# Kernel optimization log

Measured on AMD Instinct MI355X. Metric: run time of the kernel, lower is better.

Reference implementation:

```python
import jax, jax.numpy as jnp
import numpy as np

WS = 8       # window_size
SHIFT = 4    # shift_size
HEADS = 4

def _rel_pos_index():
    coords = np.stack(np.meshgrid(np.arange(WS), np.arange(WS), indexing='ij'))
    cf = coords.reshape(2, -1)                       # (2, N)
    rel = cf[:, :, None] - cf[:, None, :]            # (2, N, N)
    rel = rel.transpose(1, 2, 0).copy()              # (N, N, 2)
    rel[:, :, 0] += WS - 1
    rel[:, :, 1] += WS - 1
    rel[:, :, 0] *= 2 * WS - 1
    return jnp.asarray(rel.sum(-1))                  # (N, N) int

REL_IDX = _rel_pos_index()

def _conv(x, w, groups=1, pad=0):
    return jax.lax.conv_general_dilated(
        x, w, (1, 1), [(pad, pad), (pad, pad)],
        feature_group_count=groups,
        dimension_numbers=('NCHW', 'OIHW', 'NCHW'))

def _dwt_haar(x):
    # single-level orthonormal Haar on non-overlapping 2x2 blocks
    B, C, H, W = x.shape
    x = x.reshape(B, C, H // 2, 2, W // 2, 2)
    a = x[:, :, :, 0, :, 0]; b = x[:, :, :, 0, :, 1]
    c = x[:, :, :, 1, :, 0]; d = x[:, :, :, 1, :, 1]
    ll = (a + b + c + d) * 0.5
    lh = (a - b + c - d) * 0.5
    hl = (a + b - c - d) * 0.5
    hh = (a - b - c + d) * 0.5
    return ll, lh, hl, hh

def _idwt_haar(ll, lh, hl, hh):
    a = (ll + lh + hl + hh) * 0.5
    b = (ll - lh + hl - hh) * 0.5
    c = (ll + lh - hl - hh) * 0.5
    d = (ll - lh - hl + hh) * 0.5
    B, C, H2, W2 = ll.shape
    x = jnp.stack([jnp.stack([a, b], -1), jnp.stack([c, d], -1)], -2)  # (B,C,H2,W2,2row,2col)
    return x.transpose(0, 1, 2, 4, 3, 5).reshape(B, C, 2 * H2, 2 * W2)

def _window_partition(x):
    B, C, H, W = x.shape
    x = x.reshape(B, C, H // WS, WS, W // WS, WS).transpose(0, 2, 4, 1, 3, 5)
    return x.reshape(-1, C, WS, WS)

def _window_reverse(w, B, H, W):
    C = w.shape[1]
    x = w.reshape(B, H // WS, W // WS, C, WS, WS).transpose(0, 3, 1, 4, 2, 5)
    return x.reshape(B, C, H, W)

def setup_inputs() -> dict:
    key = jax.random.key(0)
    ks = jax.random.split(key, 8)
    dim = 64
    s = 0.05
    return {
        'x': jax.random.normal(ks[0], (8, dim, 256, 256), jnp.float32),
        'temperature': jnp.ones((HEADS, 1, 1), jnp.float32),
        'rel_bias_table': jax.random.normal(ks[1], ((2 * WS - 1) ** 2, HEADS), jnp.float32) * 0.02,
        'w_high1': jax.random.normal(ks[2], (2 * dim, dim, 3, 3), jnp.float32) * s,
        'w_high2': jax.random.normal(ks[3], (dim, 2 * dim, 1, 1), jnp.float32) * s,
        'w_highout': jax.random.normal(ks[4], (3 * dim, dim, 3, 3), jnp.float32) * s,
        'w_qkv': jax.random.normal(ks[5], (3 * dim, dim, 1, 1), jnp.float32) * s,
        'w_dwconv': jax.random.normal(ks[6], (3 * dim, 1, 3, 3), jnp.float32) * s,
        'w_proj': jax.random.normal(ks[7], (dim, dim, 1, 1), jnp.float32) * s,
    }

def reference(x, temperature, rel_bias_table, w_high1, w_high2, w_highout, w_qkv, w_dwconv, w_proj):
    B, C, H, W = x.shape
    ll, lh, hl, hh = _dwt_haar(x)
    # high-frequency modulation of v
    filt = jax.nn.relu(_conv(jnp.concatenate([lh, hl], 1), w_high1, groups=2, pad=1))
    filt = jax.nn.relu(_conv(filt, w_high2))
    qkv = _conv(_conv(ll, w_qkv), w_dwconv, groups=3 * C, pad=1)
    v_inp = qkv[:, 2 * C:]  # note: q,k from qkv are dead in the source; q=k come from shifted LL
    v = v_inp * filt + v_inp
    xs = jnp.roll(ll, (-SHIFT, -SHIFT), (2, 3))
    qw = _window_partition(xs)
    vw = _window_partition(v)
    Bw = qw.shape[0]; hd = C // HEADS; N = WS * WS
    q = qw.reshape(Bw, HEADS, hd, N)
    vv = vw.reshape(Bw, HEADS, hd, N)
    qn = q / jnp.maximum(jnp.linalg.norm(q, axis=-2, keepdims=True), 1e-12)
    # k == q in the source, so kn == qn
    attn = jnp.einsum('bhdn,bhdm->bhnm', qn, qn)                      # (Bw,h,N,N)
    bias = rel_bias_table[REL_IDX.reshape(-1)].reshape(N, N, HEADS).transpose(2, 0, 1)
    attn = (attn + bias[None]) * temperature[None]
    attn = jax.nn.softmax(attn, axis=-1)
    out = jnp.einsum('bhdm,bhnm->bhdn', vv, attn)                     # v @ attn^T
    out = out.reshape(Bw, C, WS, WS)
    out = _window_reverse(out, B, H // 2, W // 2)
    out = jnp.roll(out, (SHIFT, SHIFT), (2, 3))
    out = _conv(out, w_proj)
    yh = jax.nn.relu(_conv(jnp.concatenate([lh, hl, hh], 1), w_highout, groups=3, pad=1))
    lh2, hl2, hh2 = yh[:, :C], yh[:, C:2 * C], yh[:, 2 * C:]
    return _idwt_haar(out, lh2, hl2, hh2)
```

## Files before the change

### kernel.cpp

```cpp
#include <hip/hip_runtime.h>
#include <cstddef>

constexpr int HP  = 128 * 128;
constexpr long long S = 8LL * 64 * HP;

using short8 = __attribute__((ext_vector_type(8))) short;
using f32x4  = __attribute__((ext_vector_type(4))) float;

__device__ __forceinline__ unsigned short f2bf(float x) {
    union { float f; unsigned int u; } v{x};
    unsigned int r = v.u + 0x7FFFu + ((v.u >> 16) & 1u);
    return (unsigned short)(r >> 16);
}

__global__ __launch_bounds__(256) void k_dwt_fused(
        const float* __restrict__ x, float* __restrict__ ll,
        unsigned short* __restrict__ Tlh, unsigned short* __restrict__ Thl,
        unsigned short* __restrict__ Thh) {
    __shared__ unsigned short tlh[64][66];
    __shared__ unsigned short thl[64][66];
    __shared__ unsigned short thh[64][66];
    int b = blockIdx.y;
    int p0 = blockIdx.x * 64;
    int i = p0 >> 7, j0 = p0 & 127;
    int tid = threadIdx.x;
    {
        int p = tid & 63, c4 = tid >> 6;
        int j = j0 + p;
        const float* xb = x + (size_t)b * 64 * 65536;
#pragma unroll
        for (int k = 0; k < 16; ++k) {
            int c = c4 * 16 + k;
            const float* xp = xb + (size_t)c * 65536;
            float2 top = *(const float2*)(xp + (2 * i) * 256 + 2 * j);
            float2 bot = *(const float2*)(xp + (2 * i + 1) * 256 + 2 * j);
            float a = top.x, bb = top.y, cc = bot.x, dd = bot.y;
            ll[((size_t)b * 64 + c) * HP + p0 + p] = (a + bb + cc + dd) * 0.5f;
            tlh[c][p] = f2bf((a - bb + cc - dd) * 0.5f);
            thl[c][p] = f2bf((a + bb - cc - dd) * 0.5f);
            thh[c][p] = f2bf((a - bb - cc + dd) * 0.5f);
        }
    }
    __syncthreads();
    {
        int c = tid & 63, pq = tid >> 6;
        size_t ob = ((size_t)b * HP + p0) * 64;
#pragma unroll
        for (int k = 0; k < 16; ++k) {
            int p = pq * 16 + k;
            Tlh[ob + (size_t)p * 64 + c] = tlh[c][p];
            Thl[ob + (size_t)p * 64 + c] = thl[c][p];
            Thh[ob + (size_t)p * 64 + c] = thh[c][p];
        }
    }
}

__global__ __launch_bounds__(256) void k_wreorder(const float* __restrict__ w,
                                                  unsigned short* __restrict__ wr, int total) {
    int idx = blockIdx.x * 256 + threadIdx.x;
    if (idx >= total) return;
    int oc = idx / 576, rem = idx - oc * 576;
    int s = rem >> 6, ic = rem & 63;
    wr[idx] = f2bf(w[(oc * 64 + ic) * 9 + s]);
}

__global__ __launch_bounds__(256) void k_bias(const float* __restrict__ table,
                                              const float* __restrict__ temp,
                                              float* __restrict__ bd) {
    int idx = blockIdx.x * 256 + threadIdx.x;
    int h = idx >> 12, m = (idx >> 6) & 63, n = idx & 63;
    int i1 = n >> 3, j1 = n & 7, i2 = m >> 3, j2 = m & 7;
    int rel = (i1 - i2 + 7) * 15 + (j1 - j2 + 7);
    bd[idx] = table[rel * 4 + h] * temp[h];
}

#define ISTR 72
__global__ __launch_bounds__(256, 2) void k_conv3x3_mfma(
        const unsigned short* __restrict__ in,
        const unsigned short* __restrict__ wr,
        float* __restrict__ out, int out_ctot) {
    __shared__ __align__(16) unsigned short lin[324 * ISTR];
    __shared__ __align__(16) unsigned short lw[64 * ISTR];

    int tid = threadIdx.x;
    int b = blockIdx.y;
    int ty0 = (blockIdx.x >> 3) * 16, tx0 = (blockIdx.x & 7) * 16;

    const unsigned short* inb = in + (size_t)b * HP * 64;
    for (int idx = tid; idx < 324 * 8; idx += 256) {
        int pr = idx >> 3, l8 = idx & 7;
        int py = pr / 18, px = pr - py * 18;
        int gy = ty0 + py - 1, gx = tx0 + px - 1;
        uint4 v = make_uint4(0, 0, 0, 0);
        if (gy >= 0 && gy < 128 && gx >= 0 && gx < 128)
            v = *(const uint4*)(inb + ((size_t)(gy * 128 + gx)) * 64 + l8 * 8);
        *(uint4*)&lin[pr * ISTR + l8 * 8] = v;
    }

    int wv = tid >> 6;
    int lane = tid & 63;
    int n16 = lane & 15, quad = lane >> 4;

    f32x4 acc[4][4];
#pragma unroll
    for (int mt = 0; mt < 4; ++mt)
#pragma unroll
        for (int nt = 0; nt < 4; ++nt) acc[mt][nt] = (f32x4){0.f, 0.f, 0.f, 0.f};

    for (int s = 0; s < 9; ++s) {
        __syncthreads();
        for (int idx = tid; idx < 512; idx += 256) {
            int oc = idx >> 3, l8 = idx & 7;
            *(uint4*)&lw[oc * ISTR + l8 * 8] =
                *(const uint4*)(wr + oc * 576 + s * 64 + l8 * 8);
        }
        __syncthreads();
        int sy = s / 3, sx = s - sy * 3;
#pragma unroll
        for (int half = 0; half < 2; ++half) {
            int ic0 = half * 32 + quad * 8;
            short8 a[4], bf[4];
#pragma unroll
            for (int mt = 0; mt < 4; ++mt)
                a[mt] = *(const short8*)&lw[(mt * 16 + n16) * ISTR + ic0];
#pragma unroll
            for (int nt = 0; nt < 4; ++nt) {
                int py = 4 * wv + nt + sy;
                int px = n16 + sx;
                bf[nt] = *(const short8*)&lin[(py * 18 + px) * ISTR + ic0];
            }
#pragma unroll
            for (int mt = 0; mt < 4; ++mt)
#pragma unroll
                for (int nt = 0; nt < 4; ++nt)
                    acc[mt][nt] = __builtin_amdgcn_mfma_f32_16x16x32_bf16(
                        a[mt], bf[nt], acc[mt][nt], 0, 0, 0);
        }
    }

    int gx = tx0 + n16;
#pragma unroll
    for (int nt = 0; nt < 4; ++nt) {
        int gy = ty0 + 4 * wv + nt;
#pragma unroll
        for (int mt = 0; mt < 4; ++mt) {
#pragma unroll
            for (int r = 0; r < 4; ++r) {
                int oc = mt * 16 + quad * 4 + r;
                out[((size_t)b * out_ctot + oc) * HP + (size_t)gy * 128 + gx] =
                    fmaxf(acc[mt][nt][r], 0.0f);
            }
        }
    }
}

template <int IC, bool RELU>
__global__ __launch_bounds__(256) void k_conv1x1(const float* __restrict__ in,
                                                 const float* __restrict__ w,
                                                 float* __restrict__ out) {
    __shared__ float wl[IC * 16];
    int tid = threadIdx.x;
    int occ = blockIdx.y, b = blockIdx.z;
    for (int idx = tid; idx < IC * 16; idx += 256) {
        int o = idx & 15, ic = idx >> 4;
        wl[idx] = w[(occ * 16 + o) * IC + ic];
    }
    __syncthreads();
    int p = blockIdx.x * 256 + tid;
    const float* inp = in + (size_t)b * IC * HP + p;
    float acc[16] = {};
    for (int ic = 0; ic < IC; ++ic) {
        float xv = inp[(size_t)ic * HP];
#pragma unroll
        for (int o = 0; o < 16; ++o) acc[o] += xv * wl[ic * 16 + o];
    }
    float* op = out + ((size_t)b * 64 + occ * 16) * HP + p;
#pragma unroll
    for (int o = 0; o < 16; ++o) op[o * HP] = RELU ? fmaxf(acc[o], 0.0f) : acc[o];
}

__global__ __launch_bounds__(256) void k_dwconv_v(const float* __restrict__ t,
                                                  const float* __restrict__ wdw,
                                                  const float* __restrict__ filt,
                                                  float* __restrict__ v) {
    long long idx = (long long)blockIdx.x * 256 + threadIdx.x;
    if (idx >= S) return;
    int j = (int)(idx & 127);
    int i = (int)((idx >> 7) & 127);
    int c = (int)((idx >> 14) & 63);
    long long bc = idx >> 14;
    const float* tp = t + bc * HP;
    const float* wp = wdw + c * 9;
    float acc = 0.0f;
#pragma unroll
    for (int ky = 0; ky < 3; ++ky) {
        int y = i + ky - 1;
        if (y < 0 || y >= 128) continue;
#pragma unroll
        for (int kx = 0; kx < 3; ++kx) {
            int x = j + kx - 1;
            if (x < 0 || x >= 128) continue;
            acc += tp[y * 128 + x] * wp[ky * 3 + kx];
        }
    }
    float f = filt[idx];
    v[idx] = acc * (1.0f + f);
}

union F16 { float4 v4[4]; float f[16]; };

__global__ __launch_bounds__(512, 4) void k_attn2(const float* __restrict__ ll,
                                                  const float* __restrict__ v,
                                                  const float* __restrict__ bd,
                                                  const float* __restrict__ temp,
                                                  const float* __restrict__ wproj,
                                                  float* __restrict__ outbuf) {
    __shared__ __align__(16) float qs[64][132];
    __shared__ __align__(16) float vs[64][132];
    __shared__ __align__(16) float inv[4][128];
    int blk = blockIdx.x;
    int wjp = blk & 7, wi = (blk >> 3) & 15, b = blk >> 7;
    int tid = threadIdx.x;

    for (int idx = tid; idx < 2048; idx += 512) {
        int pq = idx & 31, c = idx >> 5;
        int i = pq >> 2, xq = (pq & 3) * 4;
        int w = xq >> 3;
        int col = w * 64 + i * 8 + (xq & 7);
        size_t cb = ((size_t)b * 64 + c) * HP;
        int qy = (wi * 8 + i + 4) & 127;
        int qx0 = wjp * 16 + xq + 4;
        int vy = wi * 8 + i, vx0 = wjp * 16 + xq;
        float4 qv;
        if (qx0 <= 124) {
            qv = *(const float4*)(ll + cb + qy * 128 + qx0);
        } else {
            const float* lr = ll + cb + qy * 128;
            qv = make_float4(lr[qx0 & 127], lr[(qx0 + 1) & 127],
                             lr[(qx0 + 2) & 127], lr[(qx0 + 3) & 127]);
        }
        *(float4*)&qs[c][col] = qv;
        *(float4*)&vs[c][col] = *(const float4*)(v + cb + vy * 128 + vx0);
    }
    __syncthreads();

    int n = tid & 63;
    int hw = tid >> 6;
    int h = hw & 3, w = hw >> 2;
    int wc = w << 6;
    float tscale = temp[h];
    float q[16];
    float ss = 0.0f;
#pragma unroll
    for (int d = 0; d < 16; ++d) {
        q[d] = qs[h * 16 + d][wc + n];
        ss += q[d] * q[d];
    }
    float invn = 1.0f / fmaxf(sqrtf(ss), 1e-12f);
    inv[h][wc + n] = invn;
    float qsc = invn * tscale;
#pragma unroll
    for (int d = 0; d < 16; ++d) q[d] *= qsc;
    __syncthreads();

    const float* bh = bd + (h << 12) + n;
    float mx = -1e30f, sum = 0.0f;
    float acc[16] = {};

    for (int c0 = 0; c0 < 64; c0 += 16) {
        float bb[16];
#pragma unroll
        for (int mm = 0; mm < 16; ++mm) bb[mm] = bh[(c0 + mm) * 64];

        float p[16] = {};
#pragma unroll
        for (int d = 0; d < 16; ++d) {
            F16 A;
            const float4* qr = (const float4*)&qs[h * 16 + d][wc + c0];
            A.v4[0] = qr[0]; A.v4[1] = qr[1]; A.v4[2] = qr[2]; A.v4[3] = qr[3];
            float qd = q[d];
#pragma unroll
            for (int mm = 0; mm < 16; ++mm) p[mm] += qd * A.f[mm];
        }
        F16 I;
        const float4* ir = (const float4*)&inv[h][wc + c0];
        I.v4[0] = ir[0]; I.v4[1] = ir[1]; I.v4[2] = ir[2]; I.v4[3] = ir[3];
        float cm = -1e30f;
#pragma unroll
        for (int mm = 0; mm < 16; ++mm) {
            p[mm] = p[mm] * I.f[mm] + bb[mm];
            cm = fmaxf(cm, p[mm]);
        }

        float nm = fmaxf(mx, cm);
        float scale = __expf(mx - nm);
        sum *= scale;
#pragma unroll
        for (int mm = 0; mm < 16; ++mm) {
            p[mm] = __expf(p[mm] - nm);
            sum += p[mm];
        }
#pragma unroll
        for (int d = 0; d < 16; ++d) acc[d] *= scale;

#pragma unroll
        for (int d = 0; d < 16; ++d) {
            F16 V;
            const float4* vr = (const float4*)&vs[h * 16 + d][wc + c0];
            V.v4[0] = vr[0]; V.v4[1] = vr[1]; V.v4[2] = vr[2]; V.v4[3] = vr[3];
            float s = acc[d];
#pragma unroll
            for (int mm = 0; mm < 16; ++mm) s += p[mm] * V.f[mm];
            acc[d] = s;
        }
        mx = nm;
    }

    float rs = 1.0f / sum;
    __syncthreads();
#pragma unroll
    for (int d = 0; d < 16; ++d) qs[h * 16 + d][wc + n] = acc[d] * rs;
    float* wl = &vs[0][0];
    for (int idx = tid; idx < 4096; idx += 512) wl[idx] = wproj[idx];
    __syncthreads();

    int h2 = tid >> 7;
    int p2 = tid & 127;
    int i2 = p2 >> 4, xp = p2 & 15;
    int col = ((xp >> 3) << 6) + (i2 << 3) + (xp & 7);
    float po[16] = {};
    for (int ic0 = 0; ic0 < 64; ic0 += 4) {
        float x0 = qs[ic0 + 0][col];
        float x1 = qs[ic0 + 1][col];
        float x2 = qs[ic0 + 2][col];
        float x3 = qs[ic0 + 3][col];
#pragma unroll
        for (int o = 0; o < 16; ++o) {
            float4 wv = *(const float4*)&wl[(h2 * 16 + o) * 64 + ic0];
            po[o] += x0 * wv.x + x1 * wv.y + x2 * wv.z + x3 * wv.w;
        }
    }
    int oy = (wi * 8 + i2 + 4) & 127, ox = (wjp * 16 + xp + 4) & 127;
#pragma unroll
    for (int o = 0; o < 16; ++o)
        outbuf[((size_t)b * 64 + h2 * 16 + o) * HP + oy * 128 + ox] = po[o];
}

__global__ __launch_bounds__(256) void k_idwt(const float* __restrict__ ll, const float* __restrict__ lh,
                                              const float* __restrict__ hl, const float* __restrict__ hh,
                                              float* __restrict__ out) {
    long long idx2 = (long long)blockIdx.x * 256 + threadIdx.x;
    if (idx2 >= S / 2) return;
    int j2 = (int)(idx2 & 63);
    int i  = (int)((idx2 >> 6) & 127);
    long long bc = idx2 >> 13;
    long long base = bc * HP + i * 128 + 2 * j2;
    float2 L = *(const float2*)(ll + base);
    float2 A = *(const float2*)(lh + base);
    float2 Bv = *(const float2*)(hl + base);
    float2 D = *(const float2*)(hh + base);
    float a0 = (L.x + A.x + Bv.x + D.x) * 0.5f;
    float b0 = (L.x - A.x + Bv.x - D.x) * 0.5f;
    float c0 = (L.x + A.x - Bv.x - D.x) * 0.5f;
    float d0 = (L.x - A.x - Bv.x + D.x) * 0.5f;
    float a1 = (L.y + A.y + Bv.y + D.y) * 0.5f;
    float b1 = (L.y - A.y + Bv.y - D.y) * 0.5f;
    float c1 = (L.y + A.y - Bv.y - D.y) * 0.5f;
    float d1 = (L.y - A.y - Bv.y + D.y) * 0.5f;
    float* op = out + bc * 256 * 256;
    *(float4*)(op + (2 * i) * 256 + 4 * j2)     = make_float4(a0, b0, a1, b1);
    *(float4*)(op + (2 * i + 1) * 256 + 4 * j2) = make_float4(c0, d0, c1, d1);
}

extern "C" void kernel_launch(void* const* d_in, const int* in_sizes, int n_in,
                              void* d_out, int out_size, void* d_ws, size_t ws_size,
                              hipStream_t stream) {
    const float* x        = (const float*)d_in[0];
    const float* temp     = (const float*)d_in[1];
    const float* table    = (const float*)d_in[2];
    const float* w_high1  = (const float*)d_in[3];
    const float* w_high2  = (const float*)d_in[4];
    const float* w_highout= (const float*)d_in[5];
    const float* w_qkv    = (const float*)d_in[6];
    const float* w_dwconv = (const float*)d_in[7];
    const float* w_proj   = (const float*)d_in[8];
    float* out = (float*)d_out;

    float* ws = (float*)d_ws;
    float* s0 = ws + 0 * S;
    float* s1 = ws + 1 * S;
    float* s2 = ws + 2 * S;
    float* s3 = ws + 3 * S;
    float* s4 = ws + 4 * S;
    float* s5 = ws + 5 * S;
    float* s6 = ws + 6 * S;
    float* s7 = ws + 7 * S;
    float* s8 = ws + 8 * S;

    unsigned short* T_lh = (unsigned short*)s4;
    unsigned short* T_hl = (unsigned short*)s4 + S;
    unsigned short* T_hh = (unsigned short*)s5;
    unsigned short* w_r1 = (unsigned short*)s5 + S;
    unsigned short* w_r2 = w_r1 + 128 * 576;
    float* bd = (float*)(w_r2 + 192 * 576);

    const int nblk = (int)(S / 256);
    dim3 b256(256);

    dim3 dg(HP / 64, 8);
    k_dwt_fused<<<dg, b256, 0, stream>>>(x, s0, T_lh, T_hl, T_hh);

    k_wreorder<<<(128 * 576 + 255) / 256, b256, 0, stream>>>(w_high1, w_r1, 128 * 576);
    k_wreorder<<<(192 * 576 + 255) / 256, b256, 0, stream>>>(w_highout, w_r2, 192 * 576);
    k_bias<<<64, b256, 0, stream>>>(table, temp, bd);

    dim3 cg(64, 8);
    k_conv3x3_mfma<<<cg, b256, 0, stream>>>(T_lh, w_r1,            s1,            128);
    k_conv3x3_mfma<<<cg, b256, 0, stream>>>(T_hl, w_r1 + 64 * 576, s1 + 64 * HP,  128);

    dim3 g1(64, 4, 8);
    k_conv1x1<128, true><<<g1, b256, 0, stream>>>(s1, w_high2, s6);

    k_conv1x1<64, false><<<g1, b256, 0, stream>>>(s0, w_qkv + 128 * 64, s7);

    k_dwconv_v<<<nblk, b256, 0, stream>>>(s7, w_dwconv + 128 * 9, s6, s6);

    k_attn2<<<1024, dim3(512), 0, stream>>>(s0, s6, bd, temp, w_proj, s8);

    k_conv3x3_mfma<<<cg, b256, 0, stream>>>(T_lh, w_r2,             s1, 64);
    k_conv3x3_mfma<<<cg, b256, 0, stream>>>(T_hl, w_r2 + 64 * 576,  s2, 64);
    k_conv3x3_mfma<<<cg, b256, 0, stream>>>(T_hh, w_r2 + 128 * 576, s3, 64);

    k_idwt<<<(int)(S / 2 / 256), b256, 0, stream>>>(s8, s1, s2, s3, out);
}
```

Baseline: 608.3 us.

## Rewrite window attention and projection with bf16 MFMA instructions

After: 560.0 us. 1.09x faster.

```diff
diff --git a/kernel.cpp b/kernel.cpp
--- a/kernel.cpp
+++ b/kernel.cpp
@@ -11,6 +11,9 @@
     union { float f; unsigned int u; } v{x};
     unsigned int r = v.u + 0x7FFFu + ((v.u >> 16) & 1u);
     return (unsigned short)(r >> 16);
+}
+__device__ __forceinline__ unsigned int pkbf(float a, float b) {
+    return (unsigned int)f2bf(a) | ((unsigned int)f2bf(b) << 16);
 }
 
 __global__ __launch_bounds__(256) void k_dwt_fused(
@@ -207,30 +210,27 @@
     v[idx] = acc * (1.0f + f);
 }
 
-union F16 { float4 v4[4]; float f[16]; };
-
-__global__ __launch_bounds__(512, 4) void k_attn2(const float* __restrict__ ll,
-                                                  const float* __restrict__ v,
-                                                  const float* __restrict__ bd,
-                                                  const float* __restrict__ temp,
-                                                  const float* __restrict__ wproj,
-                                                  float* __restrict__ outbuf) {
-    __shared__ __align__(16) float qs[64][132];
-    __shared__ __align__(16) float vs[64][132];
-    __shared__ __align__(16) float inv[4][128];
+__global__ __launch_bounds__(512, 4) void k_attn_mfma(
+        const float* __restrict__ ll, const float* __restrict__ v,
+        const float* __restrict__ bd, const float* __restrict__ temp,
+        const float* __restrict__ wproj, float* __restrict__ outbuf) {
+    __shared__ __align__(16) unsigned char lds[71680];
+    float*          qf = (float*)lds;
+    unsigned short* al = (unsigned short*)lds;
+    unsigned short* qt = (unsigned short*)(lds + 34816);
+    unsigned short* vt = (unsigned short*)(lds + 53248);
+
     int blk = blockIdx.x;
     int wjp = blk & 7, wi = (blk >> 3) & 15, b = blk >> 7;
     int tid = threadIdx.x;
 
     for (int idx = tid; idx < 2048; idx += 512) {
-        int pq = idx & 31, c = idx >> 5;
+        int ch = idx >> 5, pq = idx & 31;
         int i = pq >> 2, xq = (pq & 3) * 4;
-        int w = xq >> 3;
-        int col = w * 64 + i * 8 + (xq & 7);
-        size_t cb = ((size_t)b * 64 + c) * HP;
+        int w = xq >> 3, j0 = xq & 7;
+        size_t cb = ((size_t)b * 64 + ch) * HP;
         int qy = (wi * 8 + i + 4) & 127;
         int qx0 = wjp * 16 + xq + 4;
-        int vy = wi * 8 + i, vx0 = wjp * 16 + xq;
         float4 qv;
         if (qx0 <= 124) {
             qv = *(const float4*)(ll + cb + qy * 128 + qx0);
@@ -239,111 +239,161 @@
             qv = make_float4(lr[qx0 & 127], lr[(qx0 + 1) & 127],
                              lr[(qx0 + 2) & 127], lr[(qx0 + 3) & 127]);
         }
-        *(float4*)&qs[c][col] = qv;
-        *(float4*)&vs[c][col] = *(const float4*)(v + cb + vy * 128 + vx0);
+        int np = w * 64 + i * 8 + j0;
+        qf[(np    ) * 68 + ch] = qv.x;
+        qf[(np + 1) * 68 + ch] = qv.y;
+        qf[(np + 2) * 68 + ch] = qv.z;
+        qf[(np + 3) * 68 + ch] = qv.w;
+        int vy = wi * 8 + i, vx0 = wjp * 16 + xq;
+        float4 vv = *(const float4*)(v + cb + vy * 128 + vx0);
+        *(uint2*)&vt[(w * 64 + ch) * 72 + i * 8 + j0] =
+            make_uint2(pkbf(vv.x, vv.y), pkbf(vv.z, vv.w));
     }
     __syncthreads();
 
-    int n = tid & 63;
-    int hw = tid >> 6;
-    int h = hw & 3, w = hw >> 2;
-    int wc = w << 6;
+    {
+        int px = tid >> 2, h = tid & 3;
+        const float* qr = qf + px * 68 + h * 16;
+        float4 q0 = *(const float4*)(qr);
+        float4 q1 = *(const float4*)(qr + 4);
+        float4 q2 = *(const float4*)(qr + 8);
+        float4 q3 = *(const float4*)(qr + 12);
+        float ss = q0.x*q0.x + q0.y*q0.y + q0.z*q0.z + q0.w*q0.w
+                 + q1.x*q1.x + q1.y*q1.y + q1.z*q1.z + q1.w*q1.w
+                 + q2.x*q2.x + q2.y*q2.y + q2.z*q2.z + q2.w*q2.w
+                 + q3.x*q3.x + q3.y*q3.y + q3.z*q3.z + q3.w*q3.w;
+        float invn = 1.0f / fmaxf(sqrtf(ss), 1e-12f);
+        unsigned short* qo = qt + px * 72 + h * 16;
+        *(uint4*)(qo)     = make_uint4(pkbf(q0.x*invn, q0.y*invn), pkbf(q0.z*invn, q0.w*invn),
+                                       pkbf(q1.x*invn, q1.y*invn), pkbf(q1.z*invn, q1.w*invn));
+        *(uint4*)(qo + 8) = make_uint4(pkbf(q2.x*invn, q2.y*invn), pkbf(q2.z*invn, q2.w*invn),
+                                       pkbf(q3.x*invn, q3.y*invn), pkbf(q3.z*invn, q3.w*invn));
+    }
+    __syncthreads();
+
+    int wv = tid >> 6, lane = tid & 63;
+    int h = wv & 3, w = wv >> 2;
+    int c = lane & 15, g = lane >> 4;
+
+    short8 Fq[4];
+#pragma unroll
+    for (int t = 0; t < 4; ++t) {
+        if (g < 2) Fq[t] = *(const short8*)&qt[(w * 64 + t * 16 + c) * 72 + h * 16 + 8 * g];
+        else       Fq[t] = (short8){0, 0, 0, 0, 0, 0, 0, 0};
+    }
+    f32x4 acc[4][4];
+#pragma unroll
+    for (int ta = 0; ta < 4; ++ta)
+#pragma unroll
+        for (int tb = 0; tb < 4; ++tb)
+            acc[ta][tb] = __builtin_amdgcn_mfma_f32_16x16x32_bf16(
+                Fq[ta], Fq[tb], (f32x4){0.f, 0.f, 0.f, 0.f}, 0, 0, 0);
+
     float tscale = temp[h];
-    float q[16];
-    float ss = 0.0f;
-#pragma unroll
-    for (int d = 0; d < 16; ++d) {
-        q[d] = qs[h * 16 + d][wc + n];
-        ss += q[d] * q[d];
-    }
-    float invn = 1.0f / fmaxf(sqrtf(ss), 1e-12f);
-    inv[h][wc + n] = invn;
-    float qsc = invn * tscale;
-#pragma unroll
-    for (int d = 0; d < 16; ++d) q[d] *= qsc;
+    const float* bp = bd + (h << 12) + c;
+    float mx[4] = {-1e30f, -1e30f, -1e30f, -1e30f};
+#pragma unroll
+    for (int ta = 0; ta < 4; ++ta)
+#pragma unroll
+        for (int tb = 0; tb < 4; ++tb)
+#pragma unroll
+            for (int r = 0; r < 4; ++r) {
+                float s = acc[ta][tb][r] * tscale + bp[(ta * 16 + 4 * g + r) * 64 + tb * 16];
+                acc[ta][tb][r] = s;
+                mx[tb] = fmaxf(mx[tb], s);
+            }
+#pragma unroll
+    for (int tb = 0; tb < 4; ++tb) {
+        mx[tb] = fmaxf(mx[tb], __shfl_xor(mx[tb], 16, 64));
+        mx[tb] = fmaxf(mx[tb], __shfl_xor(mx[tb], 32, 64));
+    }
+    float sum[4] = {0.f, 0.f, 0.f, 0.f};
+#pragma unroll
+    for (int ta = 0; ta < 4; ++ta)
+#pragma unroll
+        for (int tb = 0; tb < 4; ++tb)
+#pragma unroll
+            for (int r = 0; r < 4; ++r) {
+                float p = __expf(acc[ta][tb][r] - mx[tb]);
+                acc[ta][tb][r] = p;
+                sum[tb] += p;
+            }
+    float rs[4];
+#pragma unroll
+    for (int tb = 0; tb < 4; ++tb) {
+        sum[tb] += __shfl_xor(sum[tb], 16, 64);
+        sum[tb] += __shfl_xor(sum[tb], 32, 64);
+        rs[tb] = 1.0f / sum[tb];
+    }
+    unsigned int pk[4][4][2];
+#pragma unroll
+    for (int tb = 0; tb < 4; ++tb)
+#pragma unroll
+        for (int ta = 0; ta < 4; ++ta) {
+            pk[tb][ta][0] = pkbf(acc[ta][tb][0], acc[ta][tb][1]);
+            pk[tb][ta][1] = pkbf(acc[ta][tb][2], acc[ta][tb][3]);
+        }
+
+    short8 Va[2];
+#pragma unroll
+    for (int s = 0; s < 2; ++s)
+        Va[s] = *(const short8*)&vt[(w * 64 + h * 16 + c) * 72 + s * 32 + 8 * g];
+    int srcA = (2 * (g & 1)) * 16 + c;
+    int srcB = srcA + 16;
+    int sel = g >> 1;
+#pragma unroll
+    for (int tb = 0; tb < 4; ++tb) {
+        f32x4 po = {0.f, 0.f, 0.f, 0.f};
+#pragma unroll
+        for (int s = 0; s < 2; ++s) {
+            unsigned int a0 = __shfl(pk[tb][2 * s][0], srcA, 64);
+            unsigned int b0 = __shfl(pk[tb][2 * s + 1][0], srcA, 64);
+            unsigned int a1 = __shfl(pk[tb][2 * s][1], srcA, 64);
+            unsigned int b1 = __shfl(pk[tb][2 * s + 1][1], srcA, 64);
+            unsigned int a2 = __shfl(pk[tb][2 * s][0], srcB, 64);
+            unsigned int b2 = __shfl(pk[tb][2 * s + 1][0], srcB, 64);
+            unsigned int a3 = __shfl(pk[tb][2 * s][1], srcB, 64);
+            unsigned int b3 = __shfl(pk[tb][2 * s + 1][1], srcB, 64);
+            union { short8 s8; unsigned int u[4]; } Bf;
+            Bf.u[0] = sel ? b0 : a0;
+            Bf.u[1] = sel ? b1 : a1;
+            Bf.u[2] = sel ? b2 : a2;
+            Bf.u[3] = sel ? b3 : a3;
+            po = __builtin_amdgcn_mfma_f32_16x16x32_bf16(Va[s], Bf.s8, po, 0, 0, 0);
+        }
+        int px = (2 * tb + (c >> 3)) * 16 + w * 8 + (c & 7);
+        *(uint2*)&al[px * 72 + h * 16 + 4 * g] =
+            make_uint2(pkbf(po[0] * rs[tb], po[1] * rs[tb]),
+                       pkbf(po[2] * rs[tb], po[3] * rs[tb]));
+    }
     __syncthreads();
 
-    const float* bh = bd + (h << 12) + n;
-    float mx = -1e30f, sum = 0.0f;
-    float acc[16] = {};
-
-    for (int c0 = 0; c0 < 64; c0 += 16) {
-        float bb[16];
-#pragma unroll
-        for (int mm = 0; mm < 16; ++mm) bb[mm] = bh[(c0 + mm) * 64];
-
-        float p[16] = {};
-#pragma unroll
-        for (int d = 0; d < 16; ++d) {
-            F16 A;
-            const float4* qr = (const float4*)&qs[h * 16 + d][wc + c0];
-            A.v4[0] = qr[0]; A.v4[1] = qr[1]; A.v4[2] = qr[2]; A.v4[3] = qr[3];
-            float qd = q[d];
-#pragma unroll
-            for (int mm = 0; mm < 16; ++mm) p[mm] += qd * A.f[mm];
-        }
-        F16 I;
-        const float4* ir = (const float4*)&inv[h][wc + c0];
-        I.v4[0] = ir[0]; I.v4[1] = ir[1]; I.v4[2] = ir[2]; I.v4[3] = ir[3];
-        float cm = -1e30f;
-#pragma unroll
-        for (int mm = 0; mm < 16; ++mm) {
-            p[mm] = p[mm] * I.f[mm] + bb[mm];
-            cm = fmaxf(cm, p[mm]);
-        }
-
-        float nm = fmaxf(mx, cm);
-        float scale = __expf(mx - nm);
-        sum *= scale;
-#pragma unroll
-        for (int mm = 0; mm < 16; ++mm) {
-            p[mm] = __expf(p[mm] - nm);
-            sum += p[mm];
-        }
-#pragma unroll
-        for (int d = 0; d < 16; ++d) acc[d] *= scale;
-
-#pragma unroll
-        for (int d = 0; d < 16; ++d) {
-            F16 V;
-            const float4* vr = (const float4*)&vs[h * 16 + d][wc + c0];
-            V.v4[0] = vr[0]; V.v4[1] = vr[1]; V.v4[2] = vr[2]; V.v4[3] = vr[3];
-            float s = acc[d];
-#pragma unroll
-            for (int mm = 0; mm < 16; ++mm) s += p[mm] * V.f[mm];
-            acc[d] = s;
-        }
-        mx = nm;
-    }
-
-    float rs = 1.0f / sum;
-    __syncthreads();
-#pragma unroll
-    for (int d = 0; d < 16; ++d) qs[h * 16 + d][wc + n] = acc[d] * rs;
-    float* wl = &vs[0][0];
-    for (int idx = tid; idx < 4096; idx += 512) wl[idx] = wproj[idx];
-    __syncthreads();
-
-    int h2 = tid >> 7;
-    int p2 = tid & 127;
-    int i2 = p2 >> 4, xp = p2 & 15;
-    int col = ((xp >> 3) << 6) + (i2 << 3) + (xp & 7);
-    float po[16] = {};
-    for (int ic0 = 0; ic0 < 64; ic0 += 4) {
-        float x0 = qs[ic0 + 0][col];
-        float x1 = qs[ic0 + 1][col];
-        float x2 = qs[ic0 + 2][col];
-        float x3 = qs[ic0 + 3][col];
-#pragma unroll
-        for (int o = 0; o < 16; ++o) {
-            float4 wv = *(const float4*)&wl[(h2 * 16 + o) * 64 + ic0];
-            po[o] += x0 * wv.x + x1 * wv.y + x2 * wv.z + x3 * wv.w;
-        }
-    }
-    int oy = (wi * 8 + i2 + 4) & 127, ox = (wjp * 16 + xp + 4) & 127;
-#pragma unroll
-    for (int o = 0; o < 16; ++o)
-        outbuf[((size_t)b * 64 + h2 * 16 + o) * HP + oy * 128 + ox] = po[o];
+    int to = wv & 3, pq2 = wv >> 2;
+    short8 Wf[2];
+#pragma unroll
+    for (int s = 0; s < 2; ++s) {
+        const float* wr = wproj + (to * 16 + c) * 64 + s * 32 + 8 * g;
+        float4 wa = *(const float4*)(wr);
+        float4 wb = *(const float4*)(wr + 4);
+        union { short8 s8; unsigned int u[4]; } W;
+        W.u[0] = pkbf(wa.x, wa.y); W.u[1] = pkbf(wa.z, wa.w);
+        W.u[2] = pkbf(wb.x, wb.y); W.u[3] = pkbf(wb.z, wb.w);
+        Wf[s] = W.s8;
+    }
+#pragma unroll
+    for (int t5 = 0; t5 < 4; ++t5) {
+        int tp = pq2 * 4 + t5;
+        short8 B0 = *(const short8*)&al[(tp * 16 + c) * 72 + 8 * g];
+        short8 B1 = *(const short8*)&al[(tp * 16 + c) * 72 + 32 + 8 * g];
+        f32x4 po = __builtin_amdgcn_mfma_f32_16x16x32_bf16(
+            Wf[0], B0, (f32x4){0.f, 0.f, 0.f, 0.f}, 0, 0, 0);
+        po = __builtin_amdgcn_mfma_f32_16x16x32_bf16(Wf[1], B1, po, 0, 0, 0);
+        int oy = (wi * 8 + tp + 4) & 127;
+        int ox = (wjp * 16 + c + 4) & 127;
+        size_t base = ((size_t)b * 64 + to * 16 + 4 * g) * HP + (size_t)oy * 128 + ox;
+#pragma unroll
+        for (int r = 0; r < 4; ++r) outbuf[base + (size_t)r * HP] = po[r];
+    }
 }
 
 __global__ __launch_bounds__(256) void k_idwt(const float* __restrict__ ll, const float* __restrict__ lh,
@@ -425,7 +475,7 @@
 
     k_dwconv_v<<<nblk, b256, 0, stream>>>(s7, w_dwconv + 128 * 9, s6, s6);
 
-    k_attn2<<<1024, dim3(512), 0, stream>>>(s0, s6, bd, temp, w_proj, s8);
+    k_attn_mfma<<<1024, dim3(512), 0, stream>>>(s0, s6, bd, temp, w_proj, s8);
 
     k_conv3x3_mfma<<<cg, b256, 0, stream>>>(T_lh, w_r2,             s1, 64);
     k_conv3x3_mfma<<<cg, b256, 0, stream>>>(T_hl, w_r2 + 64 * 576,  s2, 64);
```
